# Kernel optimization log

Hardware: AMD Instinct MI355X
Metric: run time of the kernel (lower is better)

## Reference

```python
import jax, jax.numpy as jnp
import numpy as np

EPS = 1e-5
NUM_GROUPS = 32


def setup_inputs() -> dict:
    key = jax.random.key(0)
    ks = jax.random.split(key, 8)
    B, C, H, W = 4, 256, 64, 64
    cond_dim = 512
    s = 0.02
    return {
        "x": jax.random.normal(ks[0], (B, C, H, W), jnp.float32),
        "cond": jax.random.normal(ks[1], (B, cond_dim), jnp.float32),
        "lin_w": jax.random.normal(ks[2], (cond_dim, 2 * C), jnp.float32) * s,
        "lin_b": jnp.zeros((2 * C,), jnp.float32),
        "qkv_w": jax.random.normal(ks[3], (C, 3 * C), jnp.float32) * s,
        "qkv_b": jnp.zeros((3 * C,), jnp.float32),
        "proj_w": jax.random.normal(ks[4], (C, C), jnp.float32) * s,
        "proj_b": jnp.zeros((C,), jnp.float32),
    }


def _group_norm(x):
    # x: [B, C, H, W]; normalize per (batch, group) over (C/G, H, W)
    B, C, H, W = x.shape
    xg = x.reshape(B, NUM_GROUPS, C // NUM_GROUPS, H, W)
    mean = jnp.mean(xg, axis=(2, 3, 4), keepdims=True)
    var = jnp.var(xg, axis=(2, 3, 4), keepdims=True)
    xg = (xg - mean) * jax.lax.rsqrt(var + EPS)
    return xg.reshape(B, C, H, W)


def reference(x, cond, lin_w, lin_b, qkv_w, qkv_b, proj_w, proj_b):
    B, C, H, W = x.shape
    # AdaGroupNorm
    h = _group_norm(x)
    sb = cond @ lin_w + lin_b                       # [B, 2C]
    scale, bias = jnp.split(sb, 2, axis=-1)
    h = h * (1.0 + scale)[:, :, None, None] + bias[:, :, None, None]
    # tokens: [B, HW, C]
    t = h.reshape(B, C, H * W).transpose(0, 2, 1)
    qkv = t @ qkv_w + qkv_b                          # [B, HW, 3C]
    q, k, v = jnp.split(qkv, 3, axis=-1)
    attn = jnp.einsum("bnc,bmc->bnm", q, k) / jnp.sqrt(jnp.float32(C))
    attn = jax.nn.softmax(attn, axis=-1)
    o = jnp.einsum("bnm,bmc->bnc", attn, v)          # [B, HW, C]
    o = o @ proj_w + proj_b
    o = o.transpose(0, 2, 1).reshape(B, C, H, W)
    return x + o
```

## Files before the change

### kernel.cpp

```cpp
#include <hip/hip_runtime.h>
#include <stdint.h>


#define AS1 __attribute__((address_space(1)))
#define AS3 __attribute__((address_space(3)))

typedef __attribute__((ext_vector_type(8))) short bf16x8;
typedef __attribute__((ext_vector_type(16))) float f32x16;

static __device__ __forceinline__ unsigned short bf16r(float x) {
  union { float f; unsigned u; } v; v.f = x;
  return (unsigned short)((v.u + 0x7fffu + ((v.u >> 16) & 1u)) >> 16);
}
static __device__ __forceinline__ unsigned bf16pack(float lo, float hi) {
  union { float f; unsigned u; } a, b; a.f = lo; b.f = hi;
  unsigned ua = a.u + 0x7fffu + ((a.u >> 16) & 1u);
  unsigned ub = b.u + 0x7fffu + ((b.u >> 16) & 1u);
  return (ua >> 16) | (ub & 0xffff0000u);
}
static __device__ __forceinline__ void gload16(const void* g, void* lds_uniform) {
  __builtin_amdgcn_global_load_lds((const AS1 unsigned*)g, (AS3 unsigned*)lds_uniform,
                                   16, 0, 0);
}
static __device__ __forceinline__ f32x16 mfma_bf16(bf16x8 a, bf16x8 b, f32x16 c) {
  return __builtin_amdgcn_mfma_f32_32x32x16_bf16(a, b, c, 0, 0, 0);
}

__global__ __launch_bounds__(256) void prep_kernel(
    const float* __restrict__ qkv_w, const float* __restrict__ proj_w,
    const float* __restrict__ cond, const float* __restrict__ lin_w,
    const float* __restrict__ lin_b,
    unsigned short* __restrict__ qkvwT, unsigned short* __restrict__ projwT,
    float* __restrict__ sb) {
  int bid = blockIdx.x, t = threadIdx.x;
  if (bid < 64) {
    __shared__ float tile[64][68];
    const float* src;
    unsigned short* dst;
    int srcCols, j0, c0;
    if (bid < 48) {
      src = qkv_w; dst = qkvwT; srcCols = 768;
      j0 = (bid >> 2) * 64; c0 = (bid & 3) * 64;
    } else {
      int b2 = bid - 48;
      src = proj_w; dst = projwT; srcCols = 256;
      j0 = (b2 >> 2) * 64; c0 = (b2 & 3) * 64;
    }
    int r = t >> 4, col4 = (t & 15) * 4;
#pragma unroll
    for (int q = 0; q < 4; ++q) {
      float4 v = *(const float4*)(src + (size_t)(c0 + r + q * 16) * srcCols + j0 + col4);
      *(float4*)&tile[r + q * 16][col4] = v;
    }
    __syncthreads();
    int jj = t >> 2, cc = (t & 3) * 16;
    union { unsigned short us[16]; bf16x8 v[2]; } o;
#pragma unroll
    for (int i = 0; i < 16; ++i) o.us[i] = bf16r(tile[cc + i][jj]);
    unsigned short* dp = dst + (size_t)(j0 + jj) * 256 + c0 + cc;
    *(bf16x8*)dp = o.v[0];
    *(bf16x8*)(dp + 8) = o.v[1];
  } else {
    int s = bid - 64;
    int b = s >> 1, j = (s & 1) * 256 + t;
    float acc = lin_b[j];
    const float* cp = cond + b * 512;
    const float* wp = lin_w + j;
#pragma unroll 8
    for (int kk = 0; kk < 512; ++kk) acc += cp[kk] * wp[(size_t)kk * 512];
    sb[b * 512 + j] = acc;
  }
}

__global__ __launch_bounds__(256) void gn_stats_kernel(
    const float* __restrict__ x, float* __restrict__ stats) {
  int bg = blockIdx.x;
  const float* p = x + (size_t)bg * 32768;
  float s = 0.f, ss = 0.f;
  for (int k = 0; k < 32; ++k) {
    int i = threadIdx.x * 4 + k * 1024;
    float4 v = *(const float4*)(p + i);
    s += v.x + v.y + v.z + v.w;
    ss += v.x * v.x + v.y * v.y + v.z * v.z + v.w * v.w;
  }
#pragma unroll
  for (int off = 1; off < 64; off <<= 1) {
    s += __shfl_xor(s, off, 64);
    ss += __shfl_xor(ss, off, 64);
  }
  __shared__ float red[8];
  if ((threadIdx.x & 63) == 0) {
    red[(threadIdx.x >> 6) * 2] = s;
    red[(threadIdx.x >> 6) * 2 + 1] = ss;
  }
  __syncthreads();
  if (threadIdx.x == 0) {
    float S = 0.f, SS = 0.f;
#pragma unroll
    for (int i = 0; i < 4; ++i) { S += red[i * 2]; SS += red[i * 2 + 1]; }
    float mean = S * (1.f / 32768.f);
    float var = SS * (1.f / 32768.f) - mean * mean;
    stats[bg * 2] = mean;
    stats[bg * 2 + 1] = rsqrtf(var + 1e-5f);
  }
}

__global__ __launch_bounds__(256) void gn_apply_kernel(
    const float* __restrict__ x, const float* __restrict__ stats,
    const float* __restrict__ sb, unsigned short* __restrict__ ht) {
  __shared__ __align__(16) unsigned short tile[64][72];
  int b = blockIdx.x >> 8, cb = (blockIdx.x >> 6) & 3, nb = blockIdx.x & 63;
  int t = threadIdx.x;
  int c0 = cb * 64, n0 = nb * 64;
#pragma unroll
  for (int q = 0; q < 4; ++q) {
    int r = q * 16 + (t >> 4);
    int nn = (t & 15) * 4;
    int c = c0 + r;
    float mean = stats[(b * 32 + (c >> 3)) * 2];
    float rstd = stats[(b * 32 + (c >> 3)) * 2 + 1];
    float scl = sb[b * 512 + c], bia = sb[b * 512 + 256 + c];
    float A = rstd * (1.f + scl);
    float Bp = bia - mean * A;
    float4 v = *(const float4*)(x + ((size_t)(b * 256 + c)) * 4096 + n0 + nn);
    ushort4 pk;
    pk.x = bf16r(v.x * A + Bp);
    pk.y = bf16r(v.y * A + Bp);
    pk.z = bf16r(v.z * A + Bp);
    pk.w = bf16r(v.w * A + Bp);
    *(ushort4*)&tile[r][nn] = pk;
  }
  __syncthreads();
#pragma unroll
  for (int q = 0; q < 2; ++q) {
    int n = t & 63, cbase = (t >> 6) * 8 + q * 32;
    bf16x8 outv;
#pragma unroll
    for (int j = 0; j < 8; ++j) outv[j] = (short)tile[cbase + j][n];
    *(bf16x8*)(ht + ((size_t)(b * 4096 + n0 + n)) * 256 + c0 + cbase) = outv;
  }
}

__global__ __launch_bounds__(256, 2) void qkv_gemm_kernel(
    const unsigned short* __restrict__ ht, const unsigned short* __restrict__ wT,
    const float* __restrict__ qkv_b, unsigned short* __restrict__ q_buf,
    unsigned short* __restrict__ k_buf, unsigned short* __restrict__ vt_buf) {
  __shared__ __align__(16) unsigned short lA[8192];
  __shared__ __align__(16) unsigned short lB[8192];
  int bid = blockIdx.x;
  int b = bid / 192, rem = bid % 192;
  int m0 = (rem / 6) * 128, j0 = (rem % 6) * 128;
  int tid = threadIdx.x, lane = tid & 63, w = tid >> 6;
  int wm = w >> 1, wn = w & 1, l31 = lane & 31, lh = lane >> 5;

  f32x16 acc[2][2];
#pragma unroll
  for (int i = 0; i < 2; ++i)
#pragma unroll
    for (int jj = 0; jj < 2; ++jj) acc[i][jj] = (f32x16)0.f;

  const char* htg = (const char*)ht;
  const char* wtg = (const char*)wT;

  for (int ks = 0; ks < 4; ++ks) {
    int k0 = ks * 64;
    if (ks) __syncthreads();
#pragma unroll
    for (int i = 0; i < 4; ++i) {
      int obase = (w * 4 + i) * 1024;
      int o = obase + lane * 16;
      int row = o >> 7, colb = o & 127;
      int sw = (row & 7) << 4;
      gload16(htg + (((size_t)(b * 4096 + m0 + row)) * 256 + k0) * 2 + (colb ^ sw),
              (char*)lA + obase);
      gload16(wtg + (((size_t)(j0 + row)) * 256 + k0) * 2 + (colb ^ sw),
              (char*)lB + obase);
    }
    __syncthreads();
#pragma unroll
    for (int ks16 = 0; ks16 < 4; ++ks16) {
      int colb = ks16 * 32 + lh * 16;
      bf16x8 af[2], bf[2];
#pragma unroll
      for (int ms = 0; ms < 2; ++ms) {
        int row = wm * 64 + ms * 32 + l31;
        af[ms] = *(const bf16x8*)((const char*)lA + row * 128 + (colb ^ ((row & 7) << 4)));
      }
#pragma unroll
      for (int ns = 0; ns < 2; ++ns) {
        int row = wn * 64 + ns * 32 + l31;
        bf[ns] = *(const bf16x8*)((const char*)lB + row * 128 + (colb ^ ((row & 7) << 4)));
      }
#pragma unroll
      for (int ms = 0; ms < 2; ++ms)
#pragma unroll
        for (int ns = 0; ns < 2; ++ns) acc[ms][ns] = mfma_bf16(af[ms], bf[ns], acc[ms][ns]);
    }
  }

#pragma unroll
  for (int ms = 0; ms < 2; ++ms)
#pragma unroll
    for (int ns = 0; ns < 2; ++ns) {
      int j = j0 + wn * 64 + ns * 32 + l31;
      float bias = qkv_b[j];
      if (j < 512) {
        unsigned short* dst = (j < 256) ? q_buf : k_buf;
        int jj = j & 255;
#pragma unroll
        for (int r = 0; r < 16; ++r) {
          int mrow = m0 + wm * 64 + ms * 32 + (r & 3) + 8 * (r >> 2) + 4 * lh;
          dst[((size_t)(b * 4096) + mrow) * 256 + jj] = bf16r(acc[ms][ns][r] + bias);
        }
      } else {
        int d = j - 512;
#pragma unroll
        for (int qd = 0; qd < 4; ++qd) {
          int nbase = m0 + wm * 64 + ms * 32 + 8 * qd + 4 * lh;
          ushort4 pk;
          pk.x = bf16r(acc[ms][ns][qd * 4 + 0] + bias);
          pk.y = bf16r(acc[ms][ns][qd * 4 + 1] + bias);
          pk.z = bf16r(acc[ms][ns][qd * 4 + 2] + bias);
          pk.w = bf16r(acc[ms][ns][qd * 4 + 3] + bias);
          *(ushort4*)(vt_buf + ((size_t)(b * 256) + d) * 4096 + nbase) = pk;
        }
      }
    }
}

__global__ __launch_bounds__(256, 1) void flash_kernel(
    const unsigned short* __restrict__ qb, const unsigned short* __restrict__ kb,
    const unsigned short* __restrict__ vtb, unsigned short* __restrict__ ob) {
  __shared__ __align__(16) char lds[131072];
  int bid = blockIdx.x;
  int b = bid >> 6, qt = bid & 63;
  int tid = threadIdx.x, lane = tid & 63, w = tid >> 6;
  int wq = w & 1, wk = w >> 1;
  int l31 = lane & 31, lh = lane >> 5;
  const size_t bq = (size_t)b * 4096;
  const int qrow = qt * 64 + wq * 32 + l31;

  bf16x8 qf[16];
  const unsigned short* qp = qb + (bq + qrow) * 256;
#pragma unroll
  for (int f = 0; f < 16; ++f) qf[f] = *(const bf16x8*)(qp + f * 16 + lh * 8);

  f32x16 oacc[8];
#pragma unroll
  for (int dt = 0; dt < 8; ++dt) oacc[dt] = (f32x16)0.f;
  float m = -1e30f, l = 0.f;

  char* kbase = lds + wk * 65536;
  char* vbase = kbase + 32768;
  const char* kg = (const char*)(kb + (bq + (size_t)wk * 2048) * 256);
  const char* vg = (const char*)(vtb + (size_t)b * 1048576 + (size_t)wk * 2048);
  const float sc = 0.09011168852f;

  for (int it = 0; it < 32; ++it) {
    int key0 = it * 64;
#pragma unroll
    for (int i = 0; i < 16; ++i) {
      int obase = wq * 16384 + i * 1024;
      int o = obase + lane * 16;
      {
        int row = o >> 9, colb = o & 511;
        gload16(kg + (key0 + row) * 512 + (colb ^ ((row & 7) << 4)), kbase + obase);
      }
      {
        int rd = o >> 7, cb2 = o & 127;
        gload16(vg + (size_t)rd * 8192 + key0 * 2 + (cb2 ^ ((rd & 7) << 4)),
                vbase + obase);
      }
    }
    __syncthreads();

    f32x16 sa[2];
#pragma unroll
    for (int t2 = 0; t2 < 2; ++t2) sa[t2] = (f32x16)0.f;
#pragma unroll
    for (int cc = 0; cc < 16; ++cc) {
#pragma unroll
      for (int t2 = 0; t2 < 2; ++t2) {
        int row = t2 * 32 + l31;
        int colb = cc * 32 + lh * 16;
        bf16x8 af = *(const bf16x8*)(kbase + row * 512 + (colb ^ ((row & 7) << 4)));
        sa[t2] = mfma_bf16(af, qf[cc], sa[t2]);
      }
    }

    float pv[32];
    float tm = -1e30f;
#pragma unroll
    for (int t2 = 0; t2 < 2; ++t2)
#pragma unroll
      for (int r = 0; r < 16; ++r) {
        float v = sa[t2][r] * sc;
        pv[t2 * 16 + r] = v;
        tm = fmaxf(tm, v);
      }
    tm = fmaxf(tm, __shfl_xor(tm, 32, 64));
    if (__any(tm > m + 8.0f)) {
      float mn = fmaxf(m, tm);
      float f = exp2f(m - mn);
      m = mn;
      l *= f;
      float fr[16];
#pragma unroll
      for (int r = 0; r < 16; ++r)
        fr[r] = __shfl(f, (r & 3) + 8 * (r >> 2) + 4 * lh, 64);
#pragma unroll
      for (int dt = 0; dt < 8; ++dt)
#pragma unroll
        for (int r = 0; r < 16; ++r) oacc[dt][r] *= fr[r];
    }
    float rs = 0.f;
#pragma unroll
    for (int i = 0; i < 32; ++i) {
      pv[i] = exp2f(pv[i] - m);
      rs += pv[i];
    }
    rs += __shfl_xor(rs, 32, 64);
    l += rs;

    unsigned pk[16], px[16];
#pragma unroll
    for (int q = 0; q < 16; ++q) pk[q] = bf16pack(pv[2 * q], pv[2 * q + 1]);
#pragma unroll
    for (int q = 0; q < 16; ++q) px[q] = (unsigned)__shfl_xor((int)pk[q], 32, 64);
    bf16x8 pa[4];
#pragma unroll
    for (int t2 = 0; t2 < 2; ++t2)
#pragma unroll
      for (int kk = 0; kk < 2; ++kk) {
        int L = t2 * 8 + kk * 4;
        union { unsigned u[4]; bf16x8 v; } fr;
        if (lh == 0) {
          fr.u[0] = pk[L]; fr.u[1] = pk[L + 1]; fr.u[2] = px[L]; fr.u[3] = px[L + 1];
        } else {
          fr.u[0] = px[L + 2]; fr.u[1] = px[L + 3]; fr.u[2] = pk[L + 2]; fr.u[3] = pk[L + 3];
        }
        pa[t2 * 2 + kk] = fr.v;
      }

#pragma unroll
    for (int dt = 0; dt < 8; ++dt) {
      int rowd = dt * 32 + l31;
      int sw = (rowd & 7) << 4;
#pragma unroll
      for (int t2 = 0; t2 < 2; ++t2)
#pragma unroll
        for (int kk = 0; kk < 2; ++kk) {
          int colb = t2 * 64 + kk * 32 + lh * 16;
          bf16x8 vf = *(const bf16x8*)(vbase + rowd * 128 + (colb ^ sw));
          oacc[dt] = mfma_bf16(pa[t2 * 2 + kk], vf, oacc[dt]);
        }
    }
    __syncthreads();
  }

  float* red = (float*)lds;
  if (lane < 32) {
    red[w * 32 + l31] = m;
    red[128 + w * 32 + l31] = l;
  }
  __syncthreads();
  int pw = w ^ 2;
  float m2 = red[pw * 32 + l31], l2 = red[128 + pw * 32 + l31];
  float M = fmaxf(m, m2);
  float fa = exp2f(m - M), fb = exp2f(m2 - M);
  float denom = fa * l + fb * l2;
  float coef = fa / denom;
  float cr[16];
#pragma unroll
  for (int r = 0; r < 16; ++r)
    cr[r] = __shfl(coef, (r & 3) + 8 * (r >> 2) + 4 * lh, 64);
#pragma unroll
  for (int dt = 0; dt < 8; ++dt)
#pragma unroll
    for (int r = 0; r < 16; ++r) oacc[dt][r] *= cr[r];

  float* obuf = (float*)(lds + 1024);
  __syncthreads();
  if (wk == 0) {
#pragma unroll
    for (int dt = 0; dt < 8; ++dt)
#pragma unroll
      for (int r = 0; r < 16; ++r) {
        int rr = (r & 3) + 8 * (r >> 2) + 4 * lh;
        obuf[(wq * 32 + rr) * 256 + dt * 32 + l31] = oacc[dt][r];
      }
  }
  __syncthreads();
  if (wk == 1) {
#pragma unroll
    for (int dt = 0; dt < 8; ++dt)
#pragma unroll
      for (int r = 0; r < 16; ++r) {
        int rr = (r & 3) + 8 * (r >> 2) + 4 * lh;
        float v = oacc[dt][r] + obuf[(wq * 32 + rr) * 256 + dt * 32 + l31];
        ob[(bq + qt * 64 + wq * 32 + rr) * 256 + dt * 32 + l31] = bf16r(v);
      }
  }
}

__global__ __launch_bounds__(256, 2) void proj_gemm_kernel(
    const unsigned short* __restrict__ obf, const unsigned short* __restrict__ wT,
    const float* __restrict__ proj_b, const float* __restrict__ x,
    float* __restrict__ out) {
  __shared__ __align__(16) unsigned short lA[8192];
  __shared__ __align__(16) unsigned short lB[8192];
  int bid = blockIdx.x;
  int b = bid >> 6, mt = (bid >> 1) & 31, nt = bid & 1;
  int m0 = mt * 128, j0 = nt * 128;
  int tid = threadIdx.x, lane = tid & 63, w = tid >> 6;
  int wm = w >> 1, wn = w & 1, l31 = lane & 31, lh = lane >> 5;

  f32x16 acc[2][2];
#pragma unroll
  for (int i = 0; i < 2; ++i)
#pragma unroll
    for (int jj = 0; jj < 2; ++jj) acc[i][jj] = (f32x16)0.f;

  const char* og = (const char*)obf;
  const char* wtg = (const char*)wT;

  for (int ks = 0; ks < 4; ++ks) {
    int k0 = ks * 64;
    if (ks) __syncthreads();
#pragma unroll
    for (int i = 0; i < 4; ++i) {
      int obase = (w * 4 + i) * 1024;
      int o = obase + lane * 16;
      int row = o >> 7, colb = o & 127;
      int sw = (row & 7) << 4;
      gload16(og + (((size_t)(b * 4096 + m0 + row)) * 256 + k0) * 2 + (colb ^ sw),
              (char*)lA + obase);
      gload16(wtg + (((size_t)(j0 + row)) * 256 + k0) * 2 + (colb ^ sw),
              (char*)lB + obase);
    }
    __syncthreads();
#pragma unroll
    for (int ks16 = 0; ks16 < 4; ++ks16) {
      int colb = ks16 * 32 + lh * 16;
      bf16x8 af[2], bf[2];
#pragma unroll
      for (int ms = 0; ms < 2; ++ms) {
        int row = wm * 64 + ms * 32 + l31;
        af[ms] = *(const bf16x8*)((const char*)lA + row * 128 + (colb ^ ((row & 7) << 4)));
      }
#pragma unroll
      for (int ns = 0; ns < 2; ++ns) {
        int row = wn * 64 + ns * 32 + l31;
        bf[ns] = *(const bf16x8*)((const char*)lB + row * 128 + (colb ^ ((row & 7) << 4)));
      }
#pragma unroll
      for (int ms = 0; ms < 2; ++ms)
#pragma unroll
        for (int ns = 0; ns < 2; ++ns) acc[ms][ns] = mfma_bf16(af[ms], bf[ns], acc[ms][ns]);
    }
  }

#pragma unroll
  for (int ms = 0; ms < 2; ++ms)
#pragma unroll
    for (int ns = 0; ns < 2; ++ns) {
      int j = j0 + wn * 64 + ns * 32 + l31;
      float bias = proj_b[j];
#pragma unroll
      for (int qd = 0; qd < 4; ++qd) {
        int nbase = m0 + wm * 64 + ms * 32 + 8 * qd + 4 * lh;
        size_t off = ((size_t)(b * 256) + j) * 4096 + nbase;
        float4 xr = *(const float4*)(x + off);
        float4 o4;
        o4.x = xr.x + bias + acc[ms][ns][qd * 4 + 0];
        o4.y = xr.y + bias + acc[ms][ns][qd * 4 + 1];
        o4.z = xr.z + bias + acc[ms][ns][qd * 4 + 2];
        o4.w = xr.w + bias + acc[ms][ns][qd * 4 + 3];
        *(float4*)(out + off) = o4;
      }
    }
}

extern "C" void kernel_launch(void* const* d_in, const int* in_sizes, int n_in,
                              void* d_out, int out_size, void* d_ws, size_t ws_size,
                              hipStream_t stream) {
  (void)in_sizes; (void)n_in; (void)out_size; (void)ws_size;
  const float* x      = (const float*)d_in[0];
  const float* cond   = (const float*)d_in[1];
  const float* lin_w  = (const float*)d_in[2];
  const float* lin_b  = (const float*)d_in[3];
  const float* qkv_w  = (const float*)d_in[4];
  const float* qkv_b  = (const float*)d_in[5];
  const float* proj_w = (const float*)d_in[6];
  const float* proj_b = (const float*)d_in[7];
  float* out = (float*)d_out;
  char* ws = (char*)d_ws;

  float* sb              = (float*)(ws + 0);
  float* stats           = (float*)(ws + 8192);
  unsigned short* qkvwT  = (unsigned short*)(ws + 16384);
  unsigned short* projwT = (unsigned short*)(ws + 409600);
  unsigned short* ht     = (unsigned short*)(ws + 540672);
  unsigned short* ob     = ht;
  unsigned short* q_buf  = (unsigned short*)(ws + 8929280);
  unsigned short* k_buf  = (unsigned short*)(ws + 17317888);
  unsigned short* vt_buf = (unsigned short*)(ws + 25706496);

  prep_kernel<<<72, 256, 0, stream>>>(qkv_w, proj_w, cond, lin_w, lin_b,
                                      qkvwT, projwT, sb);
  gn_stats_kernel<<<128, 256, 0, stream>>>(x, stats);
  gn_apply_kernel<<<1024, 256, 0, stream>>>(x, stats, sb, ht);
  qkv_gemm_kernel<<<768, 256, 0, stream>>>(ht, qkvwT, qkv_b, q_buf, k_buf, vt_buf);
  flash_kernel<<<256, 256, 0, stream>>>(q_buf, k_buf, vt_buf, ob);
  proj_gemm_kernel<<<256, 256, 0, stream>>>(ob, projwT, proj_b, x, out);
}
```

Measured before the change: 275.7 us.

## Double-buffer K/V tiles in LDS and split each tile across key-half waves

The attention loop now stages 64-key K/V tiles into two alternating LDS buffers, prefetching the next tile while the current one is computed, so the load-then-sync stall before compute is hidden. The old scheme gave each wave pair its own key half (2048 keys) in separate LDS regions. Now both wave pairs share one tile, each handling 32 of its keys, and the loop runs over 64 iterations. Loading is split by wave: waves 0-1 fetch K and waves 2-3 fetch V. This doubles the number of iterations and barriers and halves the MFMA work per iteration. LDS usage stays at 128KB.

```diff
diff --git a/kernel.cpp b/kernel.cpp
--- a/kernel.cpp
+++ b/kernel.cpp
@@ -250,54 +250,56 @@
   for (int dt = 0; dt < 8; ++dt) oacc[dt] = (f32x16)0.f;
   float m = -1e30f, l = 0.f;
 
-  char* kbase = lds + wk * 65536;
-  char* vbase = kbase + 32768;
-  const char* kg = (const char*)(kb + (bq + (size_t)wk * 2048) * 256);
-  const char* vg = (const char*)(vtb + (size_t)b * 1048576 + (size_t)wk * 2048);
+  const char* kg = (const char*)(kb + bq * 256);
+  const char* vg = (const char*)(vtb + (size_t)b * 1048576);
   const float sc = 0.09011168852f;
 
-  for (int it = 0; it < 32; ++it) {
-    int key0 = it * 64;
+  auto STAGE = [&](int bufsel, int it2) {
+    char* base = lds + bufsel * 65536;
+    int key0 = it2 * 64;
 #pragma unroll
     for (int i = 0; i < 16; ++i) {
-      int obase = wq * 16384 + i * 1024;
+      int obase = w * 16384 + i * 1024;
       int o = obase + lane * 16;
-      {
+      if (w < 2) {
         int row = o >> 9, colb = o & 511;
-        gload16(kg + (key0 + row) * 512 + (colb ^ ((row & 7) << 4)), kbase + obase);
-      }
-      {
-        int rd = o >> 7, cb2 = o & 127;
+        gload16(kg + (size_t)(key0 + row) * 512 + (colb ^ ((row & 7) << 4)),
+                base + obase);
+      } else {
+        int vo = o - 32768;
+        int rd = vo >> 7, cb2 = vo & 127;
         gload16(vg + (size_t)rd * 8192 + key0 * 2 + (cb2 ^ ((rd & 7) << 4)),
-                vbase + obase);
-      }
-    }
-    __syncthreads();
-
-    f32x16 sa[2];
-#pragma unroll
-    for (int t2 = 0; t2 < 2; ++t2) sa[t2] = (f32x16)0.f;
+                base + obase);
+      }
+    }
+  };
+
+  STAGE(0, 0);
+  __syncthreads();
+
+  for (int it = 0; it < 64; ++it) {
+    int cur = it & 1;
+    if (it < 63) STAGE(cur ^ 1, it + 1);
+    char* kbase = lds + cur * 65536;
+    char* vbase = kbase + 32768;
+
+    f32x16 sa = (f32x16)0.f;
 #pragma unroll
     for (int cc = 0; cc < 16; ++cc) {
-#pragma unroll
-      for (int t2 = 0; t2 < 2; ++t2) {
-        int row = t2 * 32 + l31;
-        int colb = cc * 32 + lh * 16;
-        bf16x8 af = *(const bf16x8*)(kbase + row * 512 + (colb ^ ((row & 7) << 4)));
-        sa[t2] = mfma_bf16(af, qf[cc], sa[t2]);
-      }
-    }
-
-    float pv[32];
+      int row = wk * 32 + l31;
+      int colb = cc * 32 + lh * 16;
+      bf16x8 af = *(const bf16x8*)(kbase + row * 512 + (colb ^ ((row & 7) << 4)));
+      sa = mfma_bf16(af, qf[cc], sa);
+    }
+
+    float pv[16];
     float tm = -1e30f;
 #pragma unroll
-    for (int t2 = 0; t2 < 2; ++t2)
-#pragma unroll
-      for (int r = 0; r < 16; ++r) {
-        float v = sa[t2][r] * sc;
-        pv[t2 * 16 + r] = v;
-        tm = fmaxf(tm, v);
-      }
+    for (int r = 0; r < 16; ++r) {
+      float v = sa[r] * sc;
+      pv[r] = v;
+      tm = fmaxf(tm, v);
+    }
     tm = fmaxf(tm, __shfl_xor(tm, 32, 64));
     if (__any(tm > m + 8.0f)) {
       float mn = fmaxf(m, tm);
@@ -315,45 +317,41 @@
     }
     float rs = 0.f;
 #pragma unroll
-    for (int i = 0; i < 32; ++i) {
+    for (int i = 0; i < 16; ++i) {
       pv[i] = exp2f(pv[i] - m);
       rs += pv[i];
     }
     rs += __shfl_xor(rs, 32, 64);
     l += rs;
 
-    unsigned pk[16], px[16];
-#pragma unroll
-    for (int q = 0; q < 16; ++q) pk[q] = bf16pack(pv[2 * q], pv[2 * q + 1]);
-#pragma unroll
-    for (int q = 0; q < 16; ++q) px[q] = (unsigned)__shfl_xor((int)pk[q], 32, 64);
-    bf16x8 pa[4];
-#pragma unroll
-    for (int t2 = 0; t2 < 2; ++t2)
-#pragma unroll
-      for (int kk = 0; kk < 2; ++kk) {
-        int L = t2 * 8 + kk * 4;
-        union { unsigned u[4]; bf16x8 v; } fr;
-        if (lh == 0) {
-          fr.u[0] = pk[L]; fr.u[1] = pk[L + 1]; fr.u[2] = px[L]; fr.u[3] = px[L + 1];
-        } else {
-          fr.u[0] = px[L + 2]; fr.u[1] = px[L + 3]; fr.u[2] = pk[L + 2]; fr.u[3] = pk[L + 3];
-        }
-        pa[t2 * 2 + kk] = fr.v;
-      }
+    unsigned pk[8], px[8];
+#pragma unroll
+    for (int q = 0; q < 8; ++q) pk[q] = bf16pack(pv[2 * q], pv[2 * q + 1]);
+#pragma unroll
+    for (int q = 0; q < 8; ++q) px[q] = (unsigned)__shfl_xor((int)pk[q], 32, 64);
+    bf16x8 pa[2];
+#pragma unroll
+    for (int kk = 0; kk < 2; ++kk) {
+      int L = kk * 4;
+      union { unsigned u[4]; bf16x8 v; } fr;
+      if (lh == 0) {
+        fr.u[0] = pk[L]; fr.u[1] = pk[L + 1]; fr.u[2] = px[L]; fr.u[3] = px[L + 1];
+      } else {
+        fr.u[0] = px[L + 2]; fr.u[1] = px[L + 3]; fr.u[2] = pk[L + 2]; fr.u[3] = pk[L + 3];
+      }
+      pa[kk] = fr.v;
+    }
 
 #pragma unroll
     for (int dt = 0; dt < 8; ++dt) {
       int rowd = dt * 32 + l31;
       int sw = (rowd & 7) << 4;
 #pragma unroll
-      for (int t2 = 0; t2 < 2; ++t2)
-#pragma unroll
-        for (int kk = 0; kk < 2; ++kk) {
-          int colb = t2 * 64 + kk * 32 + lh * 16;
-          bf16x8 vf = *(const bf16x8*)(vbase + rowd * 128 + (colb ^ sw));
-          oacc[dt] = mfma_bf16(pa[t2 * 2 + kk], vf, oacc[dt]);
-        }
+      for (int kk = 0; kk < 2; ++kk) {
+        int colb = wk * 64 + kk * 32 + lh * 16;
+        bf16x8 vf = *(const bf16x8*)(vbase + rowd * 128 + (colb ^ sw));
+        oacc[dt] = mfma_bf16(pa[kk], vf, oacc[dt]);
+      }
     }
     __syncthreads();
   }
```

Result: slower. 291.3 us (+5.7%).
